# Kernel optimization log

Hardware: AMD Instinct MI355X
Metric: run time of the kernel (lower is better)

## Reference

```python
import jax, jax.numpy as jnp
import numpy as np

NUM_CLASSES = 2
THRESHOLD = 0.35
NEGPOS_RATIO = 7
VARIANCES = (0.1, 0.2)
B, P, O = 64, 16800, 64  # batch, num_priors, num_objs per image


def point_form(pr):
    # cxcywh -> xyxy
    return jnp.concatenate([pr[:, :2] - pr[:, 2:] / 2, pr[:, :2] + pr[:, 2:] / 2], axis=1)


def jaccard(a, b):
    # a: [A,4] xyxy, b: [Bx,4] xyxy -> IoU [A,Bx]
    lt = jnp.maximum(a[:, None, :2], b[None, :, :2])
    rb = jnp.minimum(a[:, None, 2:], b[None, :, 2:])
    wh = jnp.clip(rb - lt, 0.0)
    inter = wh[..., 0] * wh[..., 1]
    area_a = ((a[:, 2] - a[:, 0]) * (a[:, 3] - a[:, 1]))[:, None]
    area_b = ((b[:, 2] - b[:, 0]) * (b[:, 3] - b[:, 1]))[None, :]
    return inter / (area_a + area_b - inter)


def encode(matched, priors):
    # matched xyxy [P,4], priors cxcywh [P,4]
    g_cxcy = (matched[:, :2] + matched[:, 2:]) / 2 - priors[:, :2]
    g_cxcy = g_cxcy / (VARIANCES[0] * priors[:, 2:])
    g_wh = (matched[:, 2:] - matched[:, :2]) / priors[:, 2:]
    g_wh = jnp.log(g_wh) / VARIANCES[1]
    return jnp.concatenate([g_cxcy, g_wh], axis=1)


def encode_landm(matched, priors):
    # matched [P,10] -> [P,5,2]
    m = matched.reshape(-1, 5, 2)
    g = (m - priors[:, None, :2]) / (VARIANCES[0] * priors[:, None, 2:])
    return g.reshape(-1, 10)


def match_one(truths, labels, landms, priors):
    # truths [O,4], labels [O], landms [O,10]
    overlaps = jaccard(truths, point_form(priors))  # [O,P]
    best_prior_overlap = overlaps.max(axis=1)       # per-gt best IoU
    best_prior_idx = overlaps.argmax(axis=1)
    valid_gt = best_prior_overlap >= 0.2
    best_truth_overlap = overlaps.max(axis=0)       # per-prior best IoU
    best_truth_idx = overlaps.argmax(axis=0)
    # index_fill(2) only for valid gts (best_prior_idx_filter)
    bto = best_truth_overlap.at[best_prior_idx].set(
        jnp.where(valid_gt, 2.0, best_truth_overlap[best_prior_idx]))
    # ensure every gt keeps its best prior
    bti = best_truth_idx.at[best_prior_idx].set(jnp.arange(truths.shape[0]))
    matches = truths[bti]                  # [P,4]
    conf = labels[bti]                     # [P]
    conf = jnp.where(bto < THRESHOLD, 0.0, conf)
    loc = encode(matches, priors)
    landm = encode_landm(landms[bti], priors)
    return loc, conf, landm


def smooth_l1_sum(x, mask):
    ax = jnp.abs(x)
    v = jnp.where(ax < 1.0, 0.5 * ax * ax, ax - 0.5)
    return (v * mask).sum()


def setup_inputs() -> dict:
    key = jax.random.key(0)
    k1, k2, k3, k4, k5, k6, k7, k8 = jax.random.split(key, 8)
    loc_data = jax.random.normal(k1, (B, P, 4), jnp.float32)
    conf_data = jax.random.normal(k2, (B, P, NUM_CLASSES), jnp.float32)
    landm_data = jax.random.normal(k3, (B, P, 10), jnp.float32)
    # priors: cx,cy in (0,1), w,h in (0.02,0.22)
    cxy = jax.random.uniform(k4, (P, 2), jnp.float32)
    wh = jax.random.uniform(k5, (P, 2), jnp.float32) * 0.2 + 0.02
    priors = jnp.concatenate([cxy, wh], axis=1)
    # targets: valid corner boxes + landmarks + label in {1,-1}
    xy1 = jax.random.uniform(k6, (B, O, 2), jnp.float32) * 0.6
    bwh = jax.random.uniform(k7, (B, O, 2), jnp.float32) * 0.3 + 0.05
    boxes = jnp.concatenate([xy1, xy1 + bwh], axis=-1)
    lms = jax.random.uniform(k8, (B, O, 10), jnp.float32)
    lab = jnp.where(jax.random.uniform(jax.random.fold_in(key, 9), (B, O, 1)) < 0.3, -1.0, 1.0)
    targets = jnp.concatenate([boxes, lms, lab], axis=-1)
    return {"loc_data": loc_data, "conf_data": conf_data, "landm_data": landm_data,
            "priors": priors, "targets": targets}


def reference(loc_data, conf_data, landm_data, priors, targets):
    num = loc_data.shape[0]
    num_priors = priors.shape[0]
    truths = targets[:, :, :4]
    landms = targets[:, :, 4:14]
    labels = targets[:, :, -1]
    loc_t, conf_t, landm_t = jax.vmap(match_one, in_axes=(0, 0, 0, None))(
        truths, labels, landms, priors)  # [B,P,4], [B,P], [B,P,10]

    # landmark loss over conf_t > 0
    pos1 = conf_t > 0
    num_pos_landm = pos1.astype(jnp.int32).sum(axis=1, keepdims=True)
    N1 = jnp.maximum(num_pos_landm.sum().astype(jnp.float32), 1.0)
    loss_landm = smooth_l1_sum(landm_data - landm_t, pos1[..., None].astype(landm_data.dtype))

    # localization loss over conf_t != 0 ; conf_t[pos] = 1
    pos = conf_t != 0
    conf_t01 = jnp.where(pos, 1, 0)  # int {0,1}
    loss_l = smooth_l1_sum(loc_data - loc_t, pos[..., None].astype(loc_data.dtype))

    # hard negative mining on per-prior CE loss (global-max log_sum_exp, as in source)
    batch_conf = conf_data.reshape(-1, NUM_CLASSES)
    x_max = batch_conf.max()
    lse = jnp.log(jnp.exp(batch_conf - x_max).sum(axis=1, keepdims=True)) + x_max
    gathered = jnp.take_along_axis(batch_conf, conf_t01.reshape(-1, 1), axis=1)
    loss_c = (lse - gathered).reshape(num, -1)  # [B,P]; positives NOT zeroed (as in source)
    loss_idx = jnp.argsort(-loss_c, axis=1)
    idx_rank = jnp.argsort(loss_idx, axis=1)
    num_pos = pos.astype(jnp.int32).sum(axis=1, keepdims=True)  # [B,1]
    num_neg = jnp.minimum(NEGPOS_RATIO * num_pos, num_priors - 1)
    neg = idx_rank < num_neg  # [B,P]
    neg_pos = pos | neg

    # cross-entropy (sum) over selected pos+neg priors
    logp = jax.nn.log_softmax(conf_data, axis=-1)  # [B,P,C]
    ce = -jnp.take_along_axis(logp, conf_t01[..., None], axis=-1)[..., 0]
    loss_c_final = (ce * neg_pos.astype(ce.dtype)).sum()

    N = jnp.maximum(num_pos.sum().astype(jnp.float32), 1.0)
    return (loss_l / N, loss_c_final / N, loss_landm / N1)
```

## Files before the change

kernel.cpp:

```cpp
#include <hip/hip_runtime.h>
#include <math.h>

#define BN 64
#define PN 16800
#define ON 64
#define THRESH 0.35f
#define NEGPOS 7
#define GX 66
#define NBLK (BN * GX)
#define GXB 17
#define PT 4
#define TG 4
#define KREG 17
#define TAILV (PN - 16 * 1024)
#define NBINS 4096
#define MAXM 4096

struct GAcc {
  unsigned ticket;
  float sl, slm, sc;
  int np, np1;
  unsigned pad0, pad1;
};

__device__ __forceinline__ unsigned f2key(float f) {
  unsigned u = __float_as_uint(f);
  return (u & 0x80000000u) ? ~u : (u | 0x80000000u);
}
__device__ __forceinline__ float key2f(unsigned k) {
  unsigned u = (k & 0x80000000u) ? (k & 0x7FFFFFFFu) : ~k;
  return __uint_as_float(u);
}
__device__ __forceinline__ float sl1(float d) {
  float a = fabsf(d);
  return (a < 1.f) ? 0.5f * a * a : a - 0.5f;
}

__global__ void k_best_truth(const float* __restrict__ priors,
                             const float* __restrict__ targets,
                             float* __restrict__ bto, int* __restrict__ bti,
                             GAcc* __restrict__ gacc) {
  int b = blockIdx.y;
  int tid = threadIdx.x;
  int base = blockIdx.x * 1024 + tid;
  if (blockIdx.x == 0 && b == 0 && tid < 8)
    ((unsigned*)gacc)[tid] = 0;

  __shared__ float4 tbox[ON];
  __shared__ float tarea[ON];
  if (tid < ON) {
    const float* tg = &targets[((long)b * ON + tid) * 15];
    float4 bx = make_float4(tg[0], tg[1], tg[2], tg[3]);
    tbox[tid] = bx;
    tarea[tid] = (bx.z - bx.x) * (bx.w - bx.y);
  }
  __syncthreads();

  float px1[PT], py1[PT], px2[PT], py2[PT], ab[PT];
  bool val[PT];
#pragma unroll
  for (int i = 0; i < PT; i++) {
    int p = base + 256 * i;
    val[i] = p < PN;
    float4 pr = reinterpret_cast<const float4*>(priors)[val[i] ? p : base];
    px1[i] = pr.x - pr.z * 0.5f; py1[i] = pr.y - pr.w * 0.5f;
    px2[i] = pr.x + pr.z * 0.5f; py2[i] = pr.y + pr.w * 0.5f;
    ab[i] = (px2[i] - px1[i]) * (py2[i] - py1[i]);
  }
  float bi[PT], bu[PT]; int id[PT];
#pragma unroll
  for (int i = 0; i < PT; i++) { bi[i] = -1.f; bu[i] = 1.f; id[i] = 0; }

#pragma unroll 4
  for (int t = 0; t < ON; t++) {
    float4 a = tbox[t];
    float aa = tarea[t];
#pragma unroll
    for (int i = 0; i < PT; i++) {
      float lx = fmaxf(a.x, px1[i]), ly = fmaxf(a.y, py1[i]);
      float rx = fminf(a.z, px2[i]), ry = fminf(a.w, py2[i]);
      float w = fmaxf(rx - lx, 0.f), h = fmaxf(ry - ly, 0.f);
      float inter = w * h;
      float uni = aa + ab[i] - inter;
      if (inter * bu[i] > bi[i] * uni) { bi[i] = inter; bu[i] = uni; id[i] = t; }
    }
  }
#pragma unroll
  for (int i = 0; i < PT; i++) {
    if (val[i]) {
      int p = base + 256 * i;
      bto[(long)b * PN + p] = bi[i] / bu[i];
      bti[(long)b * PN + p] = id[i];
    }
  }
}

__global__ void k_best_prior(const float* __restrict__ priors,
                             const float* __restrict__ targets,
                             float* __restrict__ bpo, int* __restrict__ bpi) {
  int bx = blockIdx.x;
  int b = bx >> 4;
  int t0 = (bx & 15) * TG;
  int tid = threadIdx.x;
  float ax1[TG], ay1[TG], ax2[TG], ay2[TG], area_a[TG];
#pragma unroll
  for (int i = 0; i < TG; i++) {
    const float* tg = &targets[((long)b * ON + t0 + i) * 15];
    ax1[i] = tg[0]; ay1[i] = tg[1]; ax2[i] = tg[2]; ay2[i] = tg[3];
    area_a[i] = (ax2[i] - ax1[i]) * (ay2[i] - ay1[i]);
  }
  float bi[TG], bu[TG]; int bp[TG];
#pragma unroll
  for (int i = 0; i < TG; i++) { bi[i] = -1.f; bu[i] = 1.f; bp[i] = 0x7FFFFFFF; }
  for (int p = tid; p < PN; p += 256) {
    float4 pr = reinterpret_cast<const float4*>(priors)[p];
    float px1 = pr.x - pr.z * 0.5f, py1 = pr.y - pr.w * 0.5f;
    float px2 = pr.x + pr.z * 0.5f, py2 = pr.y + pr.w * 0.5f;
    float area_b = (px2 - px1) * (py2 - py1);
#pragma unroll
    for (int i = 0; i < TG; i++) {
      float lx = fmaxf(ax1[i], px1), ly = fmaxf(ay1[i], py1);
      float rx = fminf(ax2[i], px2), ry = fminf(ay2[i], py2);
      float w = fmaxf(rx - lx, 0.f), h = fmaxf(ry - ly, 0.f);
      float inter = w * h;
      float uni = area_a[i] + area_b - inter;
      if (inter * bu[i] > bi[i] * uni) { bi[i] = inter; bu[i] = uni; bp[i] = p; }
    }
  }
#pragma unroll
  for (int off = 1; off < 64; off <<= 1) {
#pragma unroll
    for (int i = 0; i < TG; i++) {
      float oi = __shfl_xor(bi[i], off), ou = __shfl_xor(bu[i], off);
      int op = __shfl_xor(bp[i], off);
      float a = oi * bu[i], c = bi[i] * ou;
      if (a > c || (a == c && op < bp[i])) { bi[i] = oi; bu[i] = ou; bp[i] = op; }
    }
  }
  __shared__ float si[TG][4], su[TG][4];
  __shared__ int spx[TG][4];
  int w = tid >> 6;
  if ((tid & 63) == 0) {
#pragma unroll
    for (int i = 0; i < TG; i++) { si[i][w] = bi[i]; su[i][w] = bu[i]; spx[i][w] = bp[i]; }
  }
  __syncthreads();
  if (tid < TG) {
    float fi = si[tid][0], fu = su[tid][0]; int fp = spx[tid][0];
    for (int ww = 1; ww < 4; ww++) {
      float a = si[tid][ww] * fu, c = fi * su[tid][ww];
      if (a > c || (a == c && spx[tid][ww] < fp)) { fi = si[tid][ww]; fu = su[tid][ww]; fp = spx[tid][ww]; }
    }
    bpo[(long)b * ON + t0 + tid] = fi / fu;
    bpi[(long)b * ON + t0 + tid] = fp;
  }
}

__global__ void k_encode(const float* __restrict__ loc_data,
                         const float* __restrict__ conf_data,
                         const float* __restrict__ landm_data,
                         const float* __restrict__ priors,
                         const float* __restrict__ targets,
                         const float* __restrict__ bto, const int* __restrict__ bti,
                         const float* __restrict__ bpo, const int* __restrict__ bpi,
                         float* __restrict__ lossc, unsigned char* __restrict__ posf,
                         float* __restrict__ part_l, float* __restrict__ part_lm,
                         int* __restrict__ np_part, int* __restrict__ np1_part) {
  int b = blockIdx.y;
  int p = blockIdx.x * 256 + threadIdx.x;
  int bid = b * GX + blockIdx.x;
  __shared__ float4 tgs4[ON * 15 / 4];
  __shared__ int ovr[256];
  float* tgs = (float*)tgs4;
  if (threadIdx.x < ON * 15 / 4)
    tgs4[threadIdx.x] = reinterpret_cast<const float4*>(targets + (long)b * ON * 15)[threadIdx.x];
  ovr[threadIdx.x] = -1;
  __syncthreads();
  if (threadIdx.x < ON) {
    int t = threadIdx.x;
    int q = bpi[b * ON + t];
    int s = blockIdx.x * 256;
    if (q >= s && q < s + 256) {
      int valid = (bpo[b * ON + t] >= 0.2f) ? 1 : 0;
      atomicMax(&ovr[q - s], (t << 1) | valid);
    }
  }
  __syncthreads();

  float sum_l = 0.f, sum_lm = 0.f;
  int cp = 0, cp1 = 0;
  if (p < PN) {
    int t = bti[b * PN + p];
    float ov = bto[b * PN + p];
    int o = ovr[threadIdx.x];
    if (o >= 0) { t = o >> 1; if (o & 1) ov = 2.0f; }
    const float* tg = &tgs[t * 15];
    float label = tg[14];
    bool pos = ov >= THRESH;
    bool pos1 = pos && (label > 0.f);
    float4 pr = reinterpret_cast<const float4*>(priors)[p];
    if (pos) {
      float rz = 1.0f / pr.z, rw = 1.0f / pr.w;
      float m0 = tg[0], m1 = tg[1], m2 = tg[2], m3 = tg[3];
      float g0 = ((m0 + m2) * 0.5f - pr.x) * rz * 10.f;
      float g1 = ((m1 + m3) * 0.5f - pr.y) * rw * 10.f;
      float g2 = __logf((m2 - m0) * rz) * 5.f;
      float g3 = __logf((m3 - m1) * rw) * 5.f;
      const float* ld = &loc_data[((long)b * PN + p) * 4];
      sum_l = sl1(ld[0] - g0) + sl1(ld[1] - g1) + sl1(ld[2] - g2) + sl1(ld[3] - g3);
      cp = 1;
      if (pos1) {
        const float* lm = &landm_data[((long)b * PN + p) * 10];
#pragma unroll
        for (int i = 0; i < 5; i++) {
          float gx = (tg[4 + 2 * i] - pr.x) * rz * 10.f;
          float gy = (tg[5 + 2 * i] - pr.y) * rw * 10.f;
          sum_lm += sl1(lm[2 * i] - gx) + sl1(lm[2 * i + 1] - gy);
        }
        cp1 = 1;
      }
    }
    float2 c2 = reinterpret_cast<const float2*>(conf_data)[(long)b * PN + p];
    float m = fmaxf(c2.x, c2.y);
    float lse = m + __logf(__expf(c2.x - m) + __expf(c2.y - m));
    lossc[b * PN + p] = lse - (pos ? c2.y : c2.x);
    posf[b * PN + p] = pos ? 1 : 0;
  }
  for (int off = 32; off; off >>= 1) {
    sum_l += __shfl_down(sum_l, off);
    sum_lm += __shfl_down(sum_lm, off);
    cp += __shfl_down(cp, off);
    cp1 += __shfl_down(cp1, off);
  }
  __shared__ float sl4[4], slm4[4];
  __shared__ int sp4[4], sp14[4];
  int w = threadIdx.x >> 6;
  if ((threadIdx.x & 63) == 0) { sl4[w] = sum_l; slm4[w] = sum_lm; sp4[w] = cp; sp14[w] = cp1; }
  __syncthreads();
  if (threadIdx.x == 0) {
    part_l[bid] = sl4[0] + sl4[1] + sl4[2] + sl4[3];
    part_lm[bid] = slm4[0] + slm4[1] + slm4[2] + slm4[3];
    np_part[bid] = sp4[0] + sp4[1] + sp4[2] + sp4[3];
    np1_part[bid] = sp14[0] + sp14[1] + sp14[2] + sp14[3];
  }
}

__global__ void __launch_bounds__(1024) k_select(const float* __restrict__ lossc,
                                                 const unsigned char* __restrict__ posf,
                                                 const int* __restrict__ np_part,
                                                 const int* __restrict__ np1_part,
                                                 const float* __restrict__ part_l,
                                                 const float* __restrict__ part_lm,
                                                 GAcc* __restrict__ gacc,
                                                 float* __restrict__ out) {
  int b = blockIdx.x;
  int tid = threadIdx.x;
  int lane = tid & 63;
  int wv = tid >> 6;
  __shared__ unsigned hist[NBINS];
  __shared__ unsigned wtot[16];
  __shared__ float resv[MAXM];
  __shared__ int residx[MAXM];
  __shared__ int s_np, s_B, s_kp;
  __shared__ unsigned s_mc;
  const float* row = &lossc[(long)b * PN];
  const unsigned char* prow = &posf[(long)b * PN];

  if (tid == 0) s_np = 0;
  for (int i = tid; i < NBINS; i += 1024) hist[i] = 0;
  __syncthreads();
  if (tid < GX) atomicAdd(&s_np, np_part[b * GX + tid]);

  bool tailOk = tid < TAILV;
  float vreg[KREG];
  unsigned preg = 0;
#pragma unroll
  for (int r = 0; r < KREG - 1; r++) {
    vreg[r] = row[tid + 1024 * r];
    if (prow[tid + 1024 * r]) preg |= (1u << r);
  }
  vreg[KREG - 1] = tailOk ? row[tid + 1024 * (KREG - 1)] : -1.f;
  if (tailOk && prow[tid + 1024 * (KREG - 1)]) preg |= (1u << (KREG - 1));
  int breg[KREG];
#pragma unroll
  for (int r = 0; r < KREG; r++) {
    int q = (int)(vreg[r] * 256.0f);
    breg[r] = q < 0 ? 0 : (q > NBINS - 1 ? NBINS - 1 : q);
  }
  __syncthreads();
  int np = s_np;
  int k = NEGPOS * np;
  if (k > PN - 1) k = PN - 1;
  bool haveNeg = (k > 0);

  int B = NBINS, kp = 0, m = 0;
  bool allB = false, fallback = false;
  if (haveNeg) {
#pragma unroll
    for (int r = 0; r < KREG; r++)
      if (r < KREG - 1 || tailOk) atomicAdd(&hist[breg[r]], 1u);
    __syncthreads();
    int t4 = tid * 4;
    unsigned h0 = hist[t4], h1 = hist[t4 + 1], h2 = hist[t4 + 2], h3 = hist[t4 + 3];
    unsigned th = h0 + h1 + h2 + h3;
    unsigned v = th;
#pragma unroll
    for (int off = 1; off < 64; off <<= 1) {
      unsigned tv = (unsigned)__shfl_down((int)v, off);
      if (lane + off < 64) v += tv;
    }
    if (lane == 0) wtot[wv] = v;
    __syncthreads();
    unsigned add = 0;
    for (int w2 = wv + 1; w2 < 16; w2++) add += wtot[w2];
    unsigned S_t = v + add;
    unsigned S_next = S_t - th;
    if (S_t >= (unsigned)k && S_next < (unsigned)k) {
      unsigned run = S_next; int Bl; unsigned kpl;
      if (run + h3 >= (unsigned)k) { Bl = t4 + 3; kpl = k - run; }
      else { run += h3;
        if (run + h2 >= (unsigned)k) { Bl = t4 + 2; kpl = k - run; }
        else { run += h2;
          if (run + h1 >= (unsigned)k) { Bl = t4 + 1; kpl = k - run; }
          else { run += h1; Bl = t4; kpl = k - run; } } }
      s_B = Bl; s_kp = (int)kpl;
    }
    __syncthreads();
    B = s_B; kp = s_kp; m = (int)hist[B];
    allB = (kp == m);
    fallback = (!allB && m > MAXM);
  }

  float acc = 0.f;
  if (haveNeg && !allB && !fallback) {
    if (tid == 0) s_mc = 0;
    __syncthreads();
#pragma unroll
    for (int r = 0; r < KREG; r++) {
      if ((r < KREG - 1 || tailOk) && breg[r] == B) {
        unsigned slot = atomicAdd(&s_mc, 1u);
        resv[slot] = vreg[r];
        residx[slot] = (tid + 1024 * r) | (((preg >> r) & 1u) ? 0x40000000 : 0);
      }
    }
    __syncthreads();
    for (int i = tid; i < m; i += 1024) {
      float vi = resv[i];
      int pk = residx[i];
      int ii = pk & 0x3FFFFFFF;
      bool posi = (pk & 0x40000000) != 0;
      int rank = 0;
      for (int j = 0; j < m; j++) {
        float vj = resv[j];
        int ij = residx[j] & 0x3FFFFFFF;
        rank += (vj > vi || (vj == vi && ij < ii)) ? 1 : 0;
      }
      if (rank < kp && !posi) acc += vi;
    }
  }

  unsigned T = 0, R = 0, C = 0;
  if (fallback) {
    __shared__ unsigned s_lo, s_hi, fcnt[16];
    if (tid == 0) { s_lo = 0u; s_hi = 0xFFFFFFFFu; }
    __syncthreads();
    for (int it = 0; it < 32; it++) {
      unsigned lo = s_lo, hi = s_hi;
      unsigned mid = lo + ((hi - lo) >> 1) + ((hi - lo) & 1u);
      unsigned c = 0;
#pragma unroll
      for (int r = 0; r < KREG; r++)
        if (r < KREG - 1 || tailOk) c += (f2key(vreg[r]) >= mid) ? 1u : 0u;
#pragma unroll
      for (int o = 32; o; o >>= 1) c += (unsigned)__shfl_down((int)c, o);
      if (lane == 0) fcnt[wv] = c;
      __syncthreads();
      if (tid == 0) {
        unsigned tot = 0;
        for (int i = 0; i < 16; i++) tot += fcnt[i];
        if (tot >= (unsigned)k) s_lo = mid; else s_hi = mid - 1;
      }
      __syncthreads();
      if (s_lo >= s_hi) break;
    }
    T = s_lo;
    unsigned cg = 0, ce = 0;
#pragma unroll
    for (int r = 0; r < KREG; r++) {
      if (r < KREG - 1 || tailOk) {
        unsigned key = f2key(vreg[r]);
        cg += (key > T) ? 1u : 0u;
        ce += (key == T) ? 1u : 0u;
      }
    }
#pragma unroll
    for (int o = 32; o; o >>= 1) {
      cg += (unsigned)__shfl_down((int)cg, o);
      ce += (unsigned)__shfl_down((int)ce, o);
    }
    if (lane == 0) { fcnt[wv] = cg; wtot[wv] = ce; }
    __syncthreads();
    if (tid == 0) {
      unsigned tg2 = 0, te = 0;
      for (int i = 0; i < 16; i++) { tg2 += fcnt[i]; te += wtot[i]; }
      fcnt[0] = tg2; wtot[0] = te;
    }
    __syncthreads();
    C = wtot[0];
    R = (unsigned)k - fcnt[0];
    if (C != R && tid < 64) {
      unsigned running = 0;
      for (int base2 = 0; base2 < PN; base2 += 64) {
        int p = base2 + tid;
        bool tie = false, pos = false;
        float v2 = 0.f;
        if (p < PN) { v2 = row[p]; tie = (f2key(v2) == T); pos = prow[p] != 0; }
        unsigned long long mm = __ballot(tie);
        if (tie) {
          unsigned rank = running + (unsigned)__popcll(mm & ((1ull << tid) - 1));
          if (rank < R && !pos) acc += v2;
        }
        running += (unsigned)__popcll(mm);
      }
    }
  }

  unsigned ptc = 0;
#pragma unroll
  for (int r = 0; r < KREG; r++) {
    if (r < KREG - 1 || tailOk) {
      float v2 = vreg[r];
      bool pos = (preg >> r) & 1u;
      if (pos) acc += v2;
      else if (haveNeg) {
        if (!fallback) {
          if (breg[r] > B || (breg[r] == B && allB)) acc += v2;
        } else {
          if (f2key(v2) > T) acc += v2;
        }
      }
      if (fallback && pos && f2key(v2) == T) ptc++;
    }
  }
  for (int o = 32; o; o >>= 1) {
    acc += __shfl_down(acc, o);
    ptc += __shfl_down(ptc, o);
  }
  __shared__ float wsum[16];
  __shared__ unsigned wpt[16];
  if (lane == 0) { wsum[wv] = acc; wpt[wv] = ptc; }
  __syncthreads();

  __shared__ float s_rsl, s_rslm;
  __shared__ int s_rnp1;
  if (tid == 0) { s_rsl = 0.f; s_rslm = 0.f; s_rnp1 = 0; }
  __syncthreads();
  if (tid < GX) {
    atomicAdd(&s_rsl, part_l[b * GX + tid]);
    atomicAdd(&s_rslm, part_lm[b * GX + tid]);
    atomicAdd(&s_rnp1, np1_part[b * GX + tid]);
  }
  __syncthreads();

  if (tid == 0) {
    float tot = 0.f; unsigned pt = 0;
    for (int i = 0; i < 16; i++) { tot += wsum[i]; pt += wpt[i]; }
    if (fallback && C == R) tot += (float)(C - pt) * key2f(T);
    atomicAdd(&gacc->sc, tot);
    atomicAdd(&gacc->sl, s_rsl);
    atomicAdd(&gacc->slm, s_rslm);
    atomicAdd(&gacc->np, np);
    atomicAdd(&gacc->np1, s_rnp1);
  }
  __threadfence();
  __shared__ int lastF;
  if (tid == 0) lastF = (atomicAdd(&gacc->ticket, 1u) == (unsigned)(BN - 1)) ? 1 : 0;
  __syncthreads();
  if (lastF && tid == 0) {
    __threadfence();
    float sl = atomicAdd(&gacc->sl, 0.f);
    float slm = atomicAdd(&gacc->slm, 0.f);
    float sc = atomicAdd(&gacc->sc, 0.f);
    int tnp = atomicAdd(&gacc->np, 0);
    int tnp1 = atomicAdd(&gacc->np1, 0);
    float N = fmaxf((float)tnp, 1.f);
    float N1 = fmaxf((float)tnp1, 1.f);
    out[0] = sl / N;
    out[1] = sc / N;
    out[2] = slm / N1;
  }
}

extern "C" void kernel_launch(void* const* d_in, const int* in_sizes, int n_in,
                              void* d_out, int out_size, void* d_ws, size_t ws_size,
                              hipStream_t stream) {
  const float* loc_data = (const float*)d_in[0];
  const float* conf_data = (const float*)d_in[1];
  const float* landm_data = (const float*)d_in[2];
  const float* priors = (const float*)d_in[3];
  const float* targets = (const float*)d_in[4];
  float* out = (float*)d_out;

  char* ws = (char*)d_ws;
  const size_t SZ = (size_t)BN * PN * 4;
  size_t off = 0;
  float* lossc = (float*)(ws + off); off += SZ;
  float* bto = (float*)(ws + off); off += SZ;
  int* bti = (int*)(ws + off); off += SZ;
  unsigned char* posf = (unsigned char*)(ws + off); off += (size_t)BN * PN;
  off = (off + 15) & ~(size_t)15;
  float* bpo = (float*)(ws + off); off += (size_t)BN * ON * 4;
  int* bpi = (int*)(ws + off); off += (size_t)BN * ON * 4;
  float* part_l = (float*)(ws + off); off += NBLK * 4;
  float* part_lm = (float*)(ws + off); off += NBLK * 4;
  int* np_part = (int*)(ws + off); off += NBLK * 4;
  int* np1_part = (int*)(ws + off); off += NBLK * 4;
  GAcc* gacc = (GAcc*)(ws + off); off += sizeof(GAcc);

  dim3 gbt(GXB, BN);
  dim3 gbp(GX, BN);

  k_best_truth<<<gbt, 256, 0, stream>>>(priors, targets, bto, bti, gacc);
  k_best_prior<<<BN * (ON / TG), 256, 0, stream>>>(priors, targets, bpo, bpi);
  k_encode<<<gbp, 256, 0, stream>>>(loc_data, conf_data, landm_data, priors, targets,
                                    bto, bti, bpo, bpi, lossc, posf,
                                    part_l, part_lm, np_part, np1_part);
  k_select<<<BN, 1024, 0, stream>>>(lossc, posf, np_part, np1_part, part_l, part_lm,
                                    gacc, out);
}
```

Baseline: 218.5 us.

## Fuse per-gt best-prior search into per-prior matching kernel via LDS atomics

Removes the separate best-prior kernel, which recomputed all IoUs. The best-truth kernel now also tracks each gt's best prior, using a packed 64-bit key (IoU bits, inverted index) and shared-memory atomicMax per slab. It writes per-slab partials that the encode kernel reduces across 17 slabs. This saves one full IoU pass and a launch, at the cost of 64 LDS atomics per thread per image-slab and extra global reads in encode. Ties now resolve by the IoU quotient rather than by a cross-multiplied comparison.

```diff
diff --git a/kernel.cpp b/kernel.cpp
--- a/kernel.cpp
+++ b/kernel.cpp
@@ -10,7 +10,6 @@
 #define NBLK (BN * GX)
 #define GXB 17
 #define PT 4
-#define TG 4
 #define KREG 17
 #define TAILV (PN - 16 * 1024)
 #define NBINS 4096
@@ -36,37 +35,45 @@
   return (a < 1.f) ? 0.5f * a * a : a - 0.5f;
 }
 
-__global__ void k_best_truth(const float* __restrict__ priors,
-                             const float* __restrict__ targets,
-                             float* __restrict__ bto, int* __restrict__ bti,
-                             GAcc* __restrict__ gacc) {
+__global__ void k_match(const float* __restrict__ priors,
+                        const float* __restrict__ targets,
+                        float* __restrict__ bto, int* __restrict__ bti,
+                        unsigned long long* __restrict__ bpp,
+                        GAcc* __restrict__ gacc) {
   int b = blockIdx.y;
+  int slab = blockIdx.x;
   int tid = threadIdx.x;
-  int base = blockIdx.x * 1024 + tid;
-  if (blockIdx.x == 0 && b == 0 && tid < 8)
+  int base = slab * 1024 + tid;
+  if (slab == 0 && b == 0 && tid < 8)
     ((unsigned*)gacc)[tid] = 0;
 
   __shared__ float4 tbox[ON];
   __shared__ float tarea[ON];
+  __shared__ unsigned long long tbest[ON];
   if (tid < ON) {
     const float* tg = &targets[((long)b * ON + tid) * 15];
     float4 bx = make_float4(tg[0], tg[1], tg[2], tg[3]);
     tbox[tid] = bx;
     tarea[tid] = (bx.z - bx.x) * (bx.w - bx.y);
+    tbest[tid] = 0ull;
   }
   __syncthreads();
 
   float px1[PT], py1[PT], px2[PT], py2[PT], ab[PT];
+  int pidx[PT];
   bool val[PT];
 #pragma unroll
   for (int i = 0; i < PT; i++) {
     int p = base + 256 * i;
     val[i] = p < PN;
-    float4 pr = reinterpret_cast<const float4*>(priors)[val[i] ? p : base];
+    int pld = val[i] ? p : (PN - 1);
+    pidx[i] = p;
+    float4 pr = reinterpret_cast<const float4*>(priors)[pld];
     px1[i] = pr.x - pr.z * 0.5f; py1[i] = pr.y - pr.w * 0.5f;
     px2[i] = pr.x + pr.z * 0.5f; py2[i] = pr.y + pr.w * 0.5f;
     ab[i] = (px2[i] - px1[i]) * (py2[i] - py1[i]);
   }
+  bool anyValid = val[0];
   float bi[PT], bu[PT]; int id[PT];
 #pragma unroll
   for (int i = 0; i < PT; i++) { bi[i] = -1.f; bu[i] = 1.f; id[i] = 0; }
@@ -75,6 +82,7 @@
   for (int t = 0; t < ON; t++) {
     float4 a = tbox[t];
     float aa = tarea[t];
+    float in[PT], un[PT];
 #pragma unroll
     for (int i = 0; i < PT; i++) {
       float lx = fmaxf(a.x, px1[i]), ly = fmaxf(a.y, py1[i]);
@@ -82,78 +90,34 @@
       float w = fmaxf(rx - lx, 0.f), h = fmaxf(ry - ly, 0.f);
       float inter = w * h;
       float uni = aa + ab[i] - inter;
+      in[i] = val[i] ? inter : -1.f;
+      un[i] = val[i] ? uni : 1.f;
       if (inter * bu[i] > bi[i] * uni) { bi[i] = inter; bu[i] = uni; id[i] = t; }
+    }
+    float wi = in[0], wu = un[0]; int wp = pidx[0];
+#pragma unroll
+    for (int i = 1; i < PT; i++) {
+      if (in[i] * wu > wi * un[i]) { wi = in[i]; wu = un[i]; wp = pidx[i]; }
+    }
+    if (anyValid) {
+      float q = wi / wu;
+      unsigned long long key =
+          ((unsigned long long)(__float_as_uint(q) | 0x80000000u) << 32) |
+          (unsigned)(~wp);
+      atomicMax(&tbest[t], key);
     }
   }
 #pragma unroll
   for (int i = 0; i < PT; i++) {
     if (val[i]) {
-      int p = base + 256 * i;
+      int p = pidx[i];
       bto[(long)b * PN + p] = bi[i] / bu[i];
       bti[(long)b * PN + p] = id[i];
     }
   }
-}
-
-__global__ void k_best_prior(const float* __restrict__ priors,
-                             const float* __restrict__ targets,
-                             float* __restrict__ bpo, int* __restrict__ bpi) {
-  int bx = blockIdx.x;
-  int b = bx >> 4;
-  int t0 = (bx & 15) * TG;
-  int tid = threadIdx.x;
-  float ax1[TG], ay1[TG], ax2[TG], ay2[TG], area_a[TG];
-#pragma unroll
-  for (int i = 0; i < TG; i++) {
-    const float* tg = &targets[((long)b * ON + t0 + i) * 15];
-    ax1[i] = tg[0]; ay1[i] = tg[1]; ax2[i] = tg[2]; ay2[i] = tg[3];
-    area_a[i] = (ax2[i] - ax1[i]) * (ay2[i] - ay1[i]);
-  }
-  float bi[TG], bu[TG]; int bp[TG];
-#pragma unroll
-  for (int i = 0; i < TG; i++) { bi[i] = -1.f; bu[i] = 1.f; bp[i] = 0x7FFFFFFF; }
-  for (int p = tid; p < PN; p += 256) {
-    float4 pr = reinterpret_cast<const float4*>(priors)[p];
-    float px1 = pr.x - pr.z * 0.5f, py1 = pr.y - pr.w * 0.5f;
-    float px2 = pr.x + pr.z * 0.5f, py2 = pr.y + pr.w * 0.5f;
-    float area_b = (px2 - px1) * (py2 - py1);
-#pragma unroll
-    for (int i = 0; i < TG; i++) {
-      float lx = fmaxf(ax1[i], px1), ly = fmaxf(ay1[i], py1);
-      float rx = fminf(ax2[i], px2), ry = fminf(ay2[i], py2);
-      float w = fmaxf(rx - lx, 0.f), h = fmaxf(ry - ly, 0.f);
-      float inter = w * h;
-      float uni = area_a[i] + area_b - inter;
-      if (inter * bu[i] > bi[i] * uni) { bi[i] = inter; bu[i] = uni; bp[i] = p; }
-    }
-  }
-#pragma unroll
-  for (int off = 1; off < 64; off <<= 1) {
-#pragma unroll
-    for (int i = 0; i < TG; i++) {
-      float oi = __shfl_xor(bi[i], off), ou = __shfl_xor(bu[i], off);
-      int op = __shfl_xor(bp[i], off);
-      float a = oi * bu[i], c = bi[i] * ou;
-      if (a > c || (a == c && op < bp[i])) { bi[i] = oi; bu[i] = ou; bp[i] = op; }
-    }
-  }
-  __shared__ float si[TG][4], su[TG][4];
-  __shared__ int spx[TG][4];
-  int w = tid >> 6;
-  if ((tid & 63) == 0) {
-#pragma unroll
-    for (int i = 0; i < TG; i++) { si[i][w] = bi[i]; su[i][w] = bu[i]; spx[i][w] = bp[i]; }
-  }
-  __syncthreads();
-  if (tid < TG) {
-    float fi = si[tid][0], fu = su[tid][0]; int fp = spx[tid][0];
-    for (int ww = 1; ww < 4; ww++) {
-      float a = si[tid][ww] * fu, c = fi * su[tid][ww];
-      if (a > c || (a == c && spx[tid][ww] < fp)) { fi = si[tid][ww]; fu = su[tid][ww]; fp = spx[tid][ww]; }
-    }
-    bpo[(long)b * ON + t0 + tid] = fi / fu;
-    bpi[(long)b * ON + t0 + tid] = fp;
-  }
+  __syncthreads();
+  if (tid < ON)
+    bpp[((long)b * GXB + slab) * ON + tid] = tbest[tid];
 }
 
 __global__ void k_encode(const float* __restrict__ loc_data,
@@ -162,7 +126,7 @@
                          const float* __restrict__ priors,
                          const float* __restrict__ targets,
                          const float* __restrict__ bto, const int* __restrict__ bti,
-                         const float* __restrict__ bpo, const int* __restrict__ bpi,
+                         const unsigned long long* __restrict__ bpp,
                          float* __restrict__ lossc, unsigned char* __restrict__ posf,
                          float* __restrict__ part_l, float* __restrict__ part_lm,
                          int* __restrict__ np_part, int* __restrict__ np1_part) {
@@ -178,11 +142,18 @@
   __syncthreads();
   if (threadIdx.x < ON) {
     int t = threadIdx.x;
-    int q = bpi[b * ON + t];
-    int s = blockIdx.x * 256;
-    if (q >= s && q < s + 256) {
-      int valid = (bpo[b * ON + t] >= 0.2f) ? 1 : 0;
-      atomicMax(&ovr[q - s], (t << 1) | valid);
+    unsigned long long best = 0ull;
+#pragma unroll
+    for (int s = 0; s < GXB; s++) {
+      unsigned long long v = bpp[((long)b * GXB + s) * ON + t];
+      if (v > best) best = v;
+    }
+    float q = __uint_as_float((unsigned)(best >> 32) & 0x7FFFFFFFu);
+    int qp = (int)(~(unsigned)best);
+    int s0 = blockIdx.x * 256;
+    if (qp >= s0 && qp < s0 + 256) {
+      int valid = (q >= 0.2f) ? 1 : 0;
+      atomicMax(&ovr[qp - s0], (t << 1) | valid);
     }
   }
   __syncthreads();
@@ -509,21 +480,20 @@
   int* bti = (int*)(ws + off); off += SZ;
   unsigned char* posf = (unsigned char*)(ws + off); off += (size_t)BN * PN;
   off = (off + 15) & ~(size_t)15;
-  float* bpo = (float*)(ws + off); off += (size_t)BN * ON * 4;
-  int* bpi = (int*)(ws + off); off += (size_t)BN * ON * 4;
+  unsigned long long* bpp = (unsigned long long*)(ws + off);
+  off += (size_t)BN * GXB * ON * 8;
   float* part_l = (float*)(ws + off); off += NBLK * 4;
   float* part_lm = (float*)(ws + off); off += NBLK * 4;
   int* np_part = (int*)(ws + off); off += NBLK * 4;
   int* np1_part = (int*)(ws + off); off += NBLK * 4;
   GAcc* gacc = (GAcc*)(ws + off); off += sizeof(GAcc);
 
-  dim3 gbt(GXB, BN);
+  dim3 gmt(GXB, BN);
   dim3 gbp(GX, BN);
 
-  k_best_truth<<<gbt, 256, 0, stream>>>(priors, targets, bto, bti, gacc);
-  k_best_prior<<<BN * (ON / TG), 256, 0, stream>>>(priors, targets, bpo, bpi);
+  k_match<<<gmt, 256, 0, stream>>>(priors, targets, bto, bti, bpp, gacc);
   k_encode<<<gbp, 256, 0, stream>>>(loc_data, conf_data, landm_data, priors, targets,
-                                    bto, bti, bpo, bpi, lossc, posf,
+                                    bto, bti, bpp, lossc, posf,
                                     part_l, part_lm, np_part, np1_part);
   k_select<<<BN, 1024, 0, stream>>>(lossc, posf, np_part, np1_part, part_l, part_lm,
                                     gacc, out);
```

Result: slower. 535.5 us (+145.0%).

## Merge matching kernels into one launch and split best-prior scan across two halves

Applied to the files above, without the earlier changes.

Fuses the per-prior best-truth and per-truth best-prior kernels into a single launch, with block index selecting the role, so both run concurrently and one launch is saved. The best-prior search is split into two halves over priors, doubling its block count. Each half writes a packed 64-bit key (order-preserving IoU bits plus inverted index), and the encode kernel takes the max of the two keys. This keeps first-index tie-breaking, but the IoU is now recovered from the packed key.

```diff
diff --git a/kernel.cpp b/kernel.cpp
--- a/kernel.cpp
+++ b/kernel.cpp
@@ -9,8 +9,12 @@
 #define GX 66
 #define NBLK (BN * GX)
 #define GXB 17
+#define NBT (BN * GXB)
 #define PT 4
 #define TG 4
+#define PSPLIT 2
+#define PHALF 8400
+#define NBP2 (BN * 16 * PSPLIT)
 #define KREG 17
 #define TAILV (PN - 16 * 1024)
 #define NBINS 4096
@@ -36,123 +40,129 @@
   return (a < 1.f) ? 0.5f * a * a : a - 0.5f;
 }
 
-__global__ void k_best_truth(const float* __restrict__ priors,
-                             const float* __restrict__ targets,
-                             float* __restrict__ bto, int* __restrict__ bti,
-                             GAcc* __restrict__ gacc) {
-  int b = blockIdx.y;
+__global__ void k_match2(const float* __restrict__ priors,
+                         const float* __restrict__ targets,
+                         float* __restrict__ bto, int* __restrict__ bti,
+                         unsigned long long* __restrict__ bpp,
+                         GAcc* __restrict__ gacc) {
+  int bid = blockIdx.x;
   int tid = threadIdx.x;
-  int base = blockIdx.x * 1024 + tid;
-  if (blockIdx.x == 0 && b == 0 && tid < 8)
-    ((unsigned*)gacc)[tid] = 0;
-
-  __shared__ float4 tbox[ON];
-  __shared__ float tarea[ON];
-  if (tid < ON) {
-    const float* tg = &targets[((long)b * ON + tid) * 15];
-    float4 bx = make_float4(tg[0], tg[1], tg[2], tg[3]);
-    tbox[tid] = bx;
-    tarea[tid] = (bx.z - bx.x) * (bx.w - bx.y);
-  }
-  __syncthreads();
-
-  float px1[PT], py1[PT], px2[PT], py2[PT], ab[PT];
-  bool val[PT];
-#pragma unroll
-  for (int i = 0; i < PT; i++) {
-    int p = base + 256 * i;
-    val[i] = p < PN;
-    float4 pr = reinterpret_cast<const float4*>(priors)[val[i] ? p : base];
-    px1[i] = pr.x - pr.z * 0.5f; py1[i] = pr.y - pr.w * 0.5f;
-    px2[i] = pr.x + pr.z * 0.5f; py2[i] = pr.y + pr.w * 0.5f;
-    ab[i] = (px2[i] - px1[i]) * (py2[i] - py1[i]);
-  }
-  float bi[PT], bu[PT]; int id[PT];
-#pragma unroll
-  for (int i = 0; i < PT; i++) { bi[i] = -1.f; bu[i] = 1.f; id[i] = 0; }
+
+  if (bid < NBT) {
+    int b = bid / GXB;
+    int slab = bid - b * GXB;
+    int base = slab * 1024 + tid;
+    if (bid == 0 && tid < 8)
+      ((unsigned*)gacc)[tid] = 0;
+
+    __shared__ float4 tbox[ON];
+    __shared__ float tarea[ON];
+    if (tid < ON) {
+      const float* tg = &targets[((long)b * ON + tid) * 15];
+      float4 bx = make_float4(tg[0], tg[1], tg[2], tg[3]);
+      tbox[tid] = bx;
+      tarea[tid] = (bx.z - bx.x) * (bx.w - bx.y);
+    }
+    __syncthreads();
+
+    float px1[PT], py1[PT], px2[PT], py2[PT], ab[PT];
+    bool val[PT];
+#pragma unroll
+    for (int i = 0; i < PT; i++) {
+      int p = base + 256 * i;
+      val[i] = p < PN;
+      float4 pr = reinterpret_cast<const float4*>(priors)[val[i] ? p : base];
+      px1[i] = pr.x - pr.z * 0.5f; py1[i] = pr.y - pr.w * 0.5f;
+      px2[i] = pr.x + pr.z * 0.5f; py2[i] = pr.y + pr.w * 0.5f;
+      ab[i] = (px2[i] - px1[i]) * (py2[i] - py1[i]);
+    }
+    float bi[PT], bu[PT]; int id[PT];
+#pragma unroll
+    for (int i = 0; i < PT; i++) { bi[i] = -1.f; bu[i] = 1.f; id[i] = 0; }
 
 #pragma unroll 4
-  for (int t = 0; t < ON; t++) {
-    float4 a = tbox[t];
-    float aa = tarea[t];
+    for (int t = 0; t < ON; t++) {
+      float4 a = tbox[t];
+      float aa = tarea[t];
+#pragma unroll
+      for (int i = 0; i < PT; i++) {
+        float lx = fmaxf(a.x, px1[i]), ly = fmaxf(a.y, py1[i]);
+        float rx = fminf(a.z, px2[i]), ry = fminf(a.w, py2[i]);
+        float w = fmaxf(rx - lx, 0.f), h = fmaxf(ry - ly, 0.f);
+        float inter = w * h;
+        float uni = aa + ab[i] - inter;
+        if (inter * bu[i] > bi[i] * uni) { bi[i] = inter; bu[i] = uni; id[i] = t; }
+      }
+    }
 #pragma unroll
     for (int i = 0; i < PT; i++) {
-      float lx = fmaxf(a.x, px1[i]), ly = fmaxf(a.y, py1[i]);
-      float rx = fminf(a.z, px2[i]), ry = fminf(a.w, py2[i]);
-      float w = fmaxf(rx - lx, 0.f), h = fmaxf(ry - ly, 0.f);
-      float inter = w * h;
-      float uni = aa + ab[i] - inter;
-      if (inter * bu[i] > bi[i] * uni) { bi[i] = inter; bu[i] = uni; id[i] = t; }
-    }
-  }
-#pragma unroll
-  for (int i = 0; i < PT; i++) {
-    if (val[i]) {
-      int p = base + 256 * i;
-      bto[(long)b * PN + p] = bi[i] / bu[i];
-      bti[(long)b * PN + p] = id[i];
-    }
-  }
-}
-
-__global__ void k_best_prior(const float* __restrict__ priors,
-                             const float* __restrict__ targets,
-                             float* __restrict__ bpo, int* __restrict__ bpi) {
-  int bx = blockIdx.x;
-  int b = bx >> 4;
-  int t0 = (bx & 15) * TG;
-  int tid = threadIdx.x;
-  float ax1[TG], ay1[TG], ax2[TG], ay2[TG], area_a[TG];
-#pragma unroll
-  for (int i = 0; i < TG; i++) {
-    const float* tg = &targets[((long)b * ON + t0 + i) * 15];
-    ax1[i] = tg[0]; ay1[i] = tg[1]; ax2[i] = tg[2]; ay2[i] = tg[3];
-    area_a[i] = (ax2[i] - ax1[i]) * (ay2[i] - ay1[i]);
-  }
-  float bi[TG], bu[TG]; int bp[TG];
-#pragma unroll
-  for (int i = 0; i < TG; i++) { bi[i] = -1.f; bu[i] = 1.f; bp[i] = 0x7FFFFFFF; }
-  for (int p = tid; p < PN; p += 256) {
-    float4 pr = reinterpret_cast<const float4*>(priors)[p];
-    float px1 = pr.x - pr.z * 0.5f, py1 = pr.y - pr.w * 0.5f;
-    float px2 = pr.x + pr.z * 0.5f, py2 = pr.y + pr.w * 0.5f;
-    float area_b = (px2 - px1) * (py2 - py1);
+      if (val[i]) {
+        int p = base + 256 * i;
+        bto[(long)b * PN + p] = bi[i] / bu[i];
+        bti[(long)b * PN + p] = id[i];
+      }
+    }
+  } else {
+    int id2 = bid - NBT;
+    int b = id2 >> 5;
+    int rest = id2 & 31;
+    int g = rest >> 1;
+    int h = rest & 1;
+    int t0 = g * TG;
+    float ax1[TG], ay1[TG], ax2[TG], ay2[TG], area_a[TG];
 #pragma unroll
     for (int i = 0; i < TG; i++) {
-      float lx = fmaxf(ax1[i], px1), ly = fmaxf(ay1[i], py1);
-      float rx = fminf(ax2[i], px2), ry = fminf(ay2[i], py2);
-      float w = fmaxf(rx - lx, 0.f), h = fmaxf(ry - ly, 0.f);
-      float inter = w * h;
-      float uni = area_a[i] + area_b - inter;
-      if (inter * bu[i] > bi[i] * uni) { bi[i] = inter; bu[i] = uni; bp[i] = p; }
-    }
-  }
-#pragma unroll
-  for (int off = 1; off < 64; off <<= 1) {
-#pragma unroll
-    for (int i = 0; i < TG; i++) {
-      float oi = __shfl_xor(bi[i], off), ou = __shfl_xor(bu[i], off);
-      int op = __shfl_xor(bp[i], off);
-      float a = oi * bu[i], c = bi[i] * ou;
-      if (a > c || (a == c && op < bp[i])) { bi[i] = oi; bu[i] = ou; bp[i] = op; }
-    }
-  }
-  __shared__ float si[TG][4], su[TG][4];
-  __shared__ int spx[TG][4];
-  int w = tid >> 6;
-  if ((tid & 63) == 0) {
-#pragma unroll
-    for (int i = 0; i < TG; i++) { si[i][w] = bi[i]; su[i][w] = bu[i]; spx[i][w] = bp[i]; }
-  }
-  __syncthreads();
-  if (tid < TG) {
-    float fi = si[tid][0], fu = su[tid][0]; int fp = spx[tid][0];
-    for (int ww = 1; ww < 4; ww++) {
-      float a = si[tid][ww] * fu, c = fi * su[tid][ww];
-      if (a > c || (a == c && spx[tid][ww] < fp)) { fi = si[tid][ww]; fu = su[tid][ww]; fp = spx[tid][ww]; }
-    }
-    bpo[(long)b * ON + t0 + tid] = fi / fu;
-    bpi[(long)b * ON + t0 + tid] = fp;
+      const float* tg = &targets[((long)b * ON + t0 + i) * 15];
+      ax1[i] = tg[0]; ay1[i] = tg[1]; ax2[i] = tg[2]; ay2[i] = tg[3];
+      area_a[i] = (ax2[i] - ax1[i]) * (ay2[i] - ay1[i]);
+    }
+    float bi[TG], bu[TG]; int bp[TG];
+#pragma unroll
+    for (int i = 0; i < TG; i++) { bi[i] = -1.f; bu[i] = 1.f; bp[i] = 0x7FFFFFFF; }
+    int pend = (h + 1) * PHALF;
+    for (int p = h * PHALF + tid; p < pend; p += 256) {
+      float4 pr = reinterpret_cast<const float4*>(priors)[p];
+      float px1 = pr.x - pr.z * 0.5f, py1 = pr.y - pr.w * 0.5f;
+      float px2 = pr.x + pr.z * 0.5f, py2 = pr.y + pr.w * 0.5f;
+      float area_b = (px2 - px1) * (py2 - py1);
+#pragma unroll
+      for (int i = 0; i < TG; i++) {
+        float lx = fmaxf(ax1[i], px1), ly = fmaxf(ay1[i], py1);
+        float rx = fminf(ax2[i], px2), ry = fminf(ay2[i], py2);
+        float w = fmaxf(rx - lx, 0.f), h2 = fmaxf(ry - ly, 0.f);
+        float inter = w * h2;
+        float uni = area_a[i] + area_b - inter;
+        if (inter * bu[i] > bi[i] * uni) { bi[i] = inter; bu[i] = uni; bp[i] = p; }
+      }
+    }
+#pragma unroll
+    for (int off = 1; off < 64; off <<= 1) {
+#pragma unroll
+      for (int i = 0; i < TG; i++) {
+        float oi = __shfl_xor(bi[i], off), ou = __shfl_xor(bu[i], off);
+        int op = __shfl_xor(bp[i], off);
+        float a = oi * bu[i], c = bi[i] * ou;
+        if (a > c || (a == c && op < bp[i])) { bi[i] = oi; bu[i] = ou; bp[i] = op; }
+      }
+    }
+    __shared__ float si[TG][4], su[TG][4];
+    __shared__ int spx[TG][4];
+    int w = tid >> 6;
+    if ((tid & 63) == 0) {
+#pragma unroll
+      for (int i = 0; i < TG; i++) { si[i][w] = bi[i]; su[i][w] = bu[i]; spx[i][w] = bp[i]; }
+    }
+    __syncthreads();
+    if (tid < TG) {
+      float fi = si[tid][0], fu = su[tid][0]; int fp = spx[tid][0];
+      for (int ww = 1; ww < 4; ww++) {
+        float a = si[tid][ww] * fu, c = fi * su[tid][ww];
+        if (a > c || (a == c && spx[tid][ww] < fp)) { fi = si[tid][ww]; fu = su[tid][ww]; fp = spx[tid][ww]; }
+      }
+      float q = fi / fu;
+      unsigned long long key = ((unsigned long long)f2key(q) << 32) | (unsigned)(~fp);
+      bpp[((long)b * ON + t0 + tid) * PSPLIT + h] = key;
+    }
   }
 }
 
@@ -162,7 +172,7 @@
                          const float* __restrict__ priors,
                          const float* __restrict__ targets,
                          const float* __restrict__ bto, const int* __restrict__ bti,
-                         const float* __restrict__ bpo, const int* __restrict__ bpi,
+                         const unsigned long long* __restrict__ bpp,
                          float* __restrict__ lossc, unsigned char* __restrict__ posf,
                          float* __restrict__ part_l, float* __restrict__ part_lm,
                          int* __restrict__ np_part, int* __restrict__ np1_part) {
@@ -178,11 +188,15 @@
   __syncthreads();
   if (threadIdx.x < ON) {
     int t = threadIdx.x;
-    int q = bpi[b * ON + t];
-    int s = blockIdx.x * 256;
-    if (q >= s && q < s + 256) {
-      int valid = (bpo[b * ON + t] >= 0.2f) ? 1 : 0;
-      atomicMax(&ovr[q - s], (t << 1) | valid);
+    unsigned long long v0 = bpp[((long)b * ON + t) * PSPLIT];
+    unsigned long long v1 = bpp[((long)b * ON + t) * PSPLIT + 1];
+    unsigned long long best = v0 > v1 ? v0 : v1;
+    float q = key2f((unsigned)(best >> 32));
+    int qp = (int)(~(unsigned)best);
+    int s0 = blockIdx.x * 256;
+    if (qp >= s0 && qp < s0 + 256) {
+      int valid = (q >= 0.2f) ? 1 : 0;
+      atomicMax(&ovr[qp - s0], (t << 1) | valid);
     }
   }
   __syncthreads();
@@ -509,21 +523,19 @@
   int* bti = (int*)(ws + off); off += SZ;
   unsigned char* posf = (unsigned char*)(ws + off); off += (size_t)BN * PN;
   off = (off + 15) & ~(size_t)15;
-  float* bpo = (float*)(ws + off); off += (size_t)BN * ON * 4;
-  int* bpi = (int*)(ws + off); off += (size_t)BN * ON * 4;
+  unsigned long long* bpp = (unsigned long long*)(ws + off);
+  off += (size_t)BN * ON * PSPLIT * 8;
   float* part_l = (float*)(ws + off); off += NBLK * 4;
   float* part_lm = (float*)(ws + off); off += NBLK * 4;
   int* np_part = (int*)(ws + off); off += NBLK * 4;
   int* np1_part = (int*)(ws + off); off += NBLK * 4;
   GAcc* gacc = (GAcc*)(ws + off); off += sizeof(GAcc);
 
-  dim3 gbt(GXB, BN);
   dim3 gbp(GX, BN);
 
-  k_best_truth<<<gbt, 256, 0, stream>>>(priors, targets, bto, bti, gacc);
-  k_best_prior<<<BN * (ON / TG), 256, 0, stream>>>(priors, targets, bpo, bpi);
+  k_match2<<<NBT + NBP2, 256, 0, stream>>>(priors, targets, bto, bti, bpp, gacc);
   k_encode<<<gbp, 256, 0, stream>>>(loc_data, conf_data, landm_data, priors, targets,
-                                    bto, bti, bpo, bpi, lossc, posf,
+                                    bto, bti, bpp, lossc, posf,
                                     part_l, part_lm, np_part, np1_part);
   k_select<<<BN, 1024, 0, stream>>>(lossc, posf, np_part, np1_part, part_l, part_lm,
                                     gacc, out);
```

New measurement: 209.4 us. -4.2%, faster.
